# Performance work log

Measured on AMD Instinct MI355X. Metric: run time of the kernel, lower is better.

The kernel has to match this reference:

```python
import jax, jax.numpy as jnp
import numpy as np
from jax import lax

V, D, B, S = 50000, 300, 32, 128
H = 1024          # LSTM hidden per direction
NT = 9            # number of CRF tags
BN_EPS = 1e-5


def setup_inputs() -> dict:
    key = jax.random.key(0)
    ks = iter(jax.random.split(key, 48))
    def nrm(shape, scale=0.05):
        return jax.random.normal(next(ks), shape, dtype=jnp.float32) * scale
    inp = {}
    inp["x"] = jax.random.randint(next(ks), (B, S), 0, V)
    inp["y"] = jax.random.randint(next(ks), (B, S), 0, NT)
    inp["mask"] = jnp.ones((B, S), dtype=bool)
    inp["emb"] = nrm((V, D), 0.1)
    inp["lin1_w"] = nrm((512, D)); inp["lin1_b"] = jnp.zeros((512,), jnp.float32)
    in_sizes = [512, 2 * H, 2 * H, 2 * H]
    for l, isz in enumerate(in_sizes):
        inp[f"wih{l}"] = nrm((2, 4 * H, isz))   # [dir, 4H, in]
        inp[f"whh{l}"] = nrm((2, 4 * H, H))
        inp[f"bias{l}"] = jnp.zeros((2, 4 * H), jnp.float32)  # b_ih + b_hh combined
    inp["bn_gamma"] = jnp.ones((2 * H,), jnp.float32)
    inp["bn_beta"] = jnp.zeros((2 * H,), jnp.float32)
    inp["lin2_w"] = nrm((NT, 2 * H)); inp["lin2_b"] = jnp.zeros((NT,), jnp.float32)
    inp["crf_start"] = nrm((NT,), 0.1)
    inp["crf_end"] = nrm((NT,), 0.1)
    inp["crf_trans"] = nrm((NT, NT), 0.1)
    return inp


def _lstm_dir(xs, Wih, Whh, b):
    # xs: [S, B, in] -> hs: [S, B, H]; torch gate order i, f, g, o
    pre = jnp.einsum('sbi,gi->sbg', xs, Wih) + b  # [S,B,4H]
    h0 = jnp.zeros((xs.shape[1], Whh.shape[1]), xs.dtype)
    def step(carry, p):
        h, c = carry
        g = p + h @ Whh.T
        i, f, gg, o = jnp.split(g, 4, axis=-1)
        c = jax.nn.sigmoid(f) * c + jax.nn.sigmoid(i) * jnp.tanh(gg)
        h = jax.nn.sigmoid(o) * jnp.tanh(c)
        return (h, c), h
    _, hs = lax.scan(step, (h0, h0), pre)
    return hs


def _bilstm(xs, Wih, Whh, b):
    fwd = _lstm_dir(xs, Wih[0], Whh[0], b[0])
    bwd = _lstm_dir(xs[::-1], Wih[1], Whh[1], b[1])[::-1]
    return jnp.concatenate([fwd, bwd], axis=-1)


def _crf_llh(emis, tags, mask, start, end, trans):
    # torchcrf CRF forward, batch_first, reduction='sum'
    mf = mask.astype(emis.dtype)
    e_tag = jnp.take_along_axis(emis, tags[..., None], -1)[..., 0]  # [B,S]
    num = start[tags[:, 0]] + e_tag[:, 0]
    tr = trans[tags[:, :-1], tags[:, 1:]]                           # [B,S-1]
    num = num + jnp.sum(mf[:, 1:] * (tr + e_tag[:, 1:]), axis=1)
    lengths = mask.sum(axis=1).astype(jnp.int32)
    last_tag = jnp.take_along_axis(tags, (lengths - 1)[:, None], 1)[:, 0]
    num = num + end[last_tag]
    # forward algorithm (log-sum-exp recurrence over seq)
    alpha0 = start + emis[:, 0]                                     # [B,NT]
    seq_e = jnp.transpose(emis[:, 1:], (1, 0, 2))                   # [S-1,B,NT]
    seq_m = jnp.transpose(mask[:, 1:], (1, 0))                      # [S-1,B]
    def step(alpha, inp):
        e_t, m_t = inp
        nxt = jax.nn.logsumexp(alpha[:, :, None] + trans[None] + e_t[:, None, :], axis=1)
        return jnp.where(m_t[:, None], nxt, alpha), None
    alpha, _ = lax.scan(step, alpha0, (seq_e, seq_m))
    den = jax.nn.logsumexp(alpha + end, axis=1)
    return jnp.sum(num - den)


def reference(x, y, mask, emb, lin1_w, lin1_b,
              wih0, whh0, bias0, wih1, whh1, bias1,
              wih2, whh2, bias2, wih3, whh3, bias3,
              bn_gamma, bn_beta, lin2_w, lin2_b,
              crf_start, crf_end, crf_trans):
    h = emb[x]                          # [B,S,D]
    h = h @ lin1_w.T + lin1_b           # [B,S,512]
    hs = jnp.transpose(h, (1, 0, 2))    # [S,B,512]
    for Wih, Whh, bb in ((wih0, whh0, bias0), (wih1, whh1, bias1),
                         (wih2, whh2, bias2), (wih3, whh3, bias3)):
        hs = _bilstm(hs, Wih, Whh, bb)  # [S,B,2048]
    h = jnp.transpose(hs, (1, 0, 2))    # [B,S,2048]
    # BatchNorm1d eval (running mean 0, var 1) -> affine; ReLU; Dropout eval = id
    h = jax.nn.relu(bn_gamma * h / jnp.sqrt(jnp.float32(1.0 + BN_EPS)) + bn_beta)
    emis = h @ lin2_w.T + lin2_b        # [B,S,9]
    return _crf_llh(emis, y, mask, crf_start, crf_end, crf_trans)
```

## Files before the change

### kernel.cpp

```cpp
#include <hip/hip_runtime.h>
#include <hip/hip_bf16.h>

typedef __attribute__((ext_vector_type(8))) short short8;
typedef __attribute__((ext_vector_type(4))) float f32x4;
typedef unsigned short ushort_t;
typedef unsigned long long u64_t;

__device__ __forceinline__ ushort_t f2bf(float f) {
    __hip_bfloat16 h = __float2bfloat16(f);
    return *(ushort_t*)&h;
}
__device__ __forceinline__ float bf2f(ushort_t u) {
    union { float f; unsigned u32; } x; x.u32 = ((unsigned)u) << 16; return x.f;
}
__device__ __forceinline__ float sigmoidf_(float x) { return 1.0f / (1.0f + expf(-x)); }

__device__ __forceinline__ short8 cvt8(const float* p) {
    short8 r;
    #pragma unroll
    for (int j = 0; j < 8; j++) r[j] = (short)f2bf(p[j]);
    return r;
}

__global__ void lin1_pad(const float* __restrict__ w, ushort_t* __restrict__ d) {
    int idx = blockIdx.x * 256 + threadIdx.x;
    if (idx >= 512 * 320) return;
    int n = idx / 320, k = idx % 320;
    d[idx] = (k < 300) ? f2bf(w[n * 300 + k]) : (ushort_t)0;
}

__global__ void emb_gather(const int* __restrict__ x, const float* __restrict__ emb,
                           ushort_t* __restrict__ XE) {
    int tok = blockIdx.x;
    int s = tok >> 5, b = tok & 31;
    int row = x[b * 128 + s];
    const float* e = emb + (size_t)row * 300;
    for (int d = threadIdx.x; d < 320; d += 64)
        XE[(size_t)tok * 320 + d] = (d < 300) ? f2bf(e[d]) : (ushort_t)0;
}

template<bool WF32, bool F32OUT>
__global__ __launch_bounds__(256) void gemm_bias(
    const ushort_t* __restrict__ X, const void* __restrict__ Wv,
    const float* __restrict__ bias, void* __restrict__ Cv,
    int K, int ldx, int ldw, int ldc)
{
    __shared__ __align__(16) ushort_t As[4 * 64 * 8];
    __shared__ __align__(16) ushort_t Bs[4 * 64 * 8];
    const int tid = threadIdx.x;
    const int lane = tid & 63;
    const int w = tid >> 6;
    const int wm = w & 1, wn = w >> 1;
    const int m0 = blockIdx.x * 64, n0 = blockIdx.y * 64;
    const int mt = tid >> 6;
    const int r = lane & 15, q = lane >> 4;
    const ushort_t* xsrc = X + (size_t)(m0 + mt * 16 + r) * ldx + q * 8;
    const ushort_t* wsrcb = WF32 ? nullptr : (const ushort_t*)Wv + (size_t)(n0 + mt * 16 + r) * ldw + q * 8;
    const float*    wsrcf = WF32 ? (const float*)Wv + (size_t)(n0 + mt * 16 + r) * ldw + q * 8 : nullptr;
    f32x4 acc00 = {0,0,0,0}, acc01 = {0,0,0,0}, acc10 = {0,0,0,0}, acc11 = {0,0,0,0};
    for (int k0 = 0; k0 < K; k0 += 32) {
        __syncthreads();
        *(uint4*)&As[(mt * 64 + lane) * 8] = *(const uint4*)(xsrc + k0);
        if (WF32) {
            float tmp[8];
            *(float4*)&tmp[0] = *(const float4*)(wsrcf + k0);
            *(float4*)&tmp[4] = *(const float4*)(wsrcf + k0 + 4);
            *(short8*)&Bs[(mt * 64 + lane) * 8] = cvt8(tmp);
        } else {
            *(uint4*)&Bs[(mt * 64 + lane) * 8] = *(const uint4*)(wsrcb + k0);
        }
        __syncthreads();
        short8 a0 = *(const short8*)&As[((2 * wm    ) * 64 + lane) * 8];
        short8 a1 = *(const short8*)&As[((2 * wm + 1) * 64 + lane) * 8];
        short8 b0 = *(const short8*)&Bs[((2 * wn    ) * 64 + lane) * 8];
        short8 b1 = *(const short8*)&Bs[((2 * wn + 1) * 64 + lane) * 8];
        acc00 = __builtin_amdgcn_mfma_f32_16x16x32_bf16(a0, b0, acc00, 0, 0, 0);
        acc01 = __builtin_amdgcn_mfma_f32_16x16x32_bf16(a0, b1, acc01, 0, 0, 0);
        acc10 = __builtin_amdgcn_mfma_f32_16x16x32_bf16(a1, b0, acc10, 0, 0, 0);
        acc11 = __builtin_amdgcn_mfma_f32_16x16x32_bf16(a1, b1, acc11, 0, 0, 0);
    }
    const int mb = m0 + wm * 32, nb = n0 + wn * 32;
    f32x4 accs[2][2] = {{acc00, acc01}, {acc10, acc11}};
    for (int i = 0; i < 2; i++)
        for (int j = 0; j < 2; j++) {
            int n = nb + j * 16 + r;
            float bv = bias[n];
            #pragma unroll
            for (int reg = 0; reg < 4; reg++) {
                int m = mb + i * 16 + q * 4 + reg;
                float v = accs[i][j][reg] + bv;
                if (F32OUT) ((float*)Cv)[(size_t)m * ldc + n] = v;
                else ((ushort_t*)Cv)[(size_t)m * ldc + n] = f2bf(v);
            }
        }
}

__device__ __forceinline__ void gbar(unsigned* cnt, int dir, int& epoch) {
    __syncthreads();
    epoch++;
    if (threadIdx.x == 0) {
        unsigned* c = cnt + dir * 32;
        __hip_atomic_fetch_add(c, 1u, __ATOMIC_RELAXED, __HIP_MEMORY_SCOPE_AGENT);
        unsigned tgt = (unsigned)epoch * 32u;
        int spins = 0;
        while (__hip_atomic_load(c, __ATOMIC_RELAXED, __HIP_MEMORY_SCOPE_AGENT) < tgt) {
            __builtin_amdgcn_s_sleep(1);
            if (++spins >= 65536) {
                spins = 0;
                if (__hip_atomic_load(c, __ATOMIC_ACQUIRE, __HIP_MEMORY_SCOPE_AGENT) >= tgt)
                    break;
            }
        }
    }
    __syncthreads();
}

__global__ __launch_bounds__(512) void lstm_scan(
    const float* __restrict__ PRE,
    const float* __restrict__ WHH,
    ushort_t* __restrict__ H,
    ushort_t* __restrict__ OUT,
    unsigned* __restrict__ cnt,
    int epoch0)
{
    const int tid = threadIdx.x;
    const int lane = tid & 63;
    const int w = tid >> 6;
    const int dir = blockIdx.x >> 5;
    const int slice = blockIdx.x & 31;
    const int u0 = slice * 32;
    __shared__ __align__(16) ushort_t Af[2 * 32 * 64 * 8];
    __shared__ float gl[32 * 132];

    const int colw = w * 16 + (lane & 15);
    short8 bfr[32];
    {
        const int gate = colw >> 5, unit = colw & 31;
        const float* wrow = WHH + ((size_t)(dir * 4096 + gate * 1024 + u0 + unit)) * 1024 + (lane >> 4) * 8;
        #pragma unroll
        for (int kc = 0; kc < 32; kc++) {
            float tmp[8];
            *(float4*)&tmp[0] = *(const float4*)(wrow + kc * 32);
            *(float4*)&tmp[4] = *(const float4*)(wrow + kc * 32 + 4);
            bfr[kc] = cvt8(tmp);
        }
    }
    const int eb = tid >> 4, eu = tid & 15;
    float cst0 = 0.f, cst1 = 0.f;
    if ((eu & 1) == 0) {
        ushort_t* hz = H + (size_t)((0 * 2 + dir) * 32 + eb) * 1024 + u0;
        __hip_atomic_store((unsigned*)(hz + eu),      0u, __ATOMIC_RELAXED, __HIP_MEMORY_SCOPE_AGENT);
        __hip_atomic_store((unsigned*)(hz + 16 + eu), 0u, __ATOMIC_RELAXED, __HIP_MEMORY_SCOPE_AGENT);
    }
    int epoch = epoch0;
    gbar(cnt, dir, epoch);

    for (int t = 0; t < 128; t++) {
        const int s = dir ? (127 - t) : t;
        const int bufr = t & 1, bufw = bufr ^ 1;
        float pb[8];
        {
            const float* pp = PRE + ((size_t)(s * 32 + eb)) * 8192 + (size_t)dir * 4096 + u0 + eu;
            #pragma unroll
            for (int g = 0; g < 4; g++) {
                pb[2 * g]     = pp[g * 1024];
                pb[2 * g + 1] = pp[g * 1024 + 16];
            }
        }
        const ushort_t* Hsrc = H + (size_t)((bufr * 2 + dir) * 32) * 1024;
        u64_t tmp[16];
        #pragma unroll
        for (int i = 0; i < 8; i++) {
            int c = tid + i * 512;
            int ln = c & 63;
            int kc = (c >> 6) & 31;
            int mt2 = c >> 11;
            int b = mt2 * 16 + (ln & 15);
            int k = kc * 32 + (ln >> 4) * 8;
            const u64_t* src = (const u64_t*)(Hsrc + (size_t)b * 1024 + k);
            tmp[2 * i]     = __hip_atomic_load(src,     __ATOMIC_RELAXED, __HIP_MEMORY_SCOPE_AGENT);
            tmp[2 * i + 1] = __hip_atomic_load(src + 1, __ATOMIC_RELAXED, __HIP_MEMORY_SCOPE_AGENT);
        }
        #pragma unroll
        for (int i = 0; i < 8; i++) {
            int c = tid + i * 512;
            *(u64_t*)&Af[(size_t)c * 8]     = tmp[2 * i];
            *(u64_t*)&Af[(size_t)c * 8 + 4] = tmp[2 * i + 1];
        }
        __syncthreads();
        f32x4 acc0 = {0,0,0,0}, acc1 = {0,0,0,0};
        #pragma unroll
        for (int kc = 0; kc < 32; kc++) {
            short8 a0 = *(const short8*)&Af[(size_t)((     kc) * 64 + lane) * 8];
            short8 a1 = *(const short8*)&Af[(size_t)((32 + kc) * 64 + lane) * 8];
            acc0 = __builtin_amdgcn_mfma_f32_16x16x32_bf16(a0, bfr[kc], acc0, 0, 0, 0);
            acc1 = __builtin_amdgcn_mfma_f32_16x16x32_bf16(a1, bfr[kc], acc1, 0, 0, 0);
        }
        const int rowb = (lane >> 4) * 4;
        #pragma unroll
        for (int reg = 0; reg < 4; reg++) {
            gl[(rowb + reg) * 132 + colw]        = acc0[reg];
            gl[(16 + rowb + reg) * 132 + colw]   = acc1[reg];
        }
        __syncthreads();
        {
            float gi0 = gl[eb * 132 +  0 + eu] + pb[0];
            float gi1 = gl[eb * 132 + 16 + eu] + pb[1];
            float gf0 = gl[eb * 132 + 32 + eu] + pb[2];
            float gf1 = gl[eb * 132 + 48 + eu] + pb[3];
            float gg0 = gl[eb * 132 + 64 + eu] + pb[4];
            float gg1 = gl[eb * 132 + 80 + eu] + pb[5];
            float go0 = gl[eb * 132 + 96 + eu] + pb[6];
            float go1 = gl[eb * 132 + 112 + eu] + pb[7];
            cst0 = sigmoidf_(gf0) * cst0 + sigmoidf_(gi0) * tanhf(gg0);
            cst1 = sigmoidf_(gf1) * cst1 + sigmoidf_(gi1) * tanhf(gg1);
            float h0 = sigmoidf_(go0) * tanhf(cst0);
            float h1 = sigmoidf_(go1) * tanhf(cst1);
            ushort_t hb0 = f2bf(h0), hb1 = f2bf(h1);
            unsigned o0 = (unsigned)(ushort_t)__shfl_xor((int)(unsigned)hb0, 1);
            unsigned o1 = (unsigned)(ushort_t)__shfl_xor((int)(unsigned)hb1, 1);
            if ((eu & 1) == 0) {
                ushort_t* hw = H + (size_t)((bufw * 2 + dir) * 32 + eb) * 1024 + u0;
                __hip_atomic_store((unsigned*)(hw + eu),      (unsigned)hb0 | (o0 << 16),
                                   __ATOMIC_RELAXED, __HIP_MEMORY_SCOPE_AGENT);
                __hip_atomic_store((unsigned*)(hw + 16 + eu), (unsigned)hb1 | (o1 << 16),
                                   __ATOMIC_RELAXED, __HIP_MEMORY_SCOPE_AGENT);
            }
            ushort_t* op = OUT + ((size_t)(s * 32 + eb)) * 2048 + (size_t)dir * 1024 + u0;
            op[eu] = hb0;
            op[16 + eu] = hb1;
        }
        gbar(cnt, dir, epoch);
    }
}

__global__ void emis_kernel(const ushort_t* __restrict__ Xf,
                            const float* __restrict__ gamma, const float* __restrict__ beta,
                            const float* __restrict__ w2, const float* __restrict__ b2,
                            float* __restrict__ EM)
{
    int idx = blockIdx.x * 256 + threadIdx.x;
    if (idx >= 32 * 128 * 9) return;
    int k = idx % 9;
    int tok = idx / 9;
    int s = tok >> 5, b = tok & 31;
    const float inv = 0.9999950000374997f;
    float acc = b2[k];
    const ushort_t* xr = Xf + (size_t)tok * 2048;
    const float* wr = w2 + (size_t)k * 2048;
    for (int j = 0; j < 2048; j++) {
        float h = gamma[j] * bf2f(xr[j]) * inv + beta[j];
        h = h > 0.f ? h : 0.f;
        acc += h * wr[j];
    }
    EM[((size_t)b * 128 + s) * 9 + k] = acc;
}

__global__ __launch_bounds__(512) void crf_kernel(
    const float* __restrict__ EM,
    const int* __restrict__ y,
    const float* __restrict__ start, const float* __restrict__ endw,
    const float* __restrict__ trans,
    float* __restrict__ out)
{
    __shared__ float tr[81], st[9], en[9];
    __shared__ float alpha[2][32][12];
    __shared__ float numsh[32], densh[32];
    int tid = threadIdx.x;
    if (tid < 81) tr[tid] = trans[tid];
    if (tid < 9) { st[tid] = start[tid]; en[tid] = endw[tid]; }
    __syncthreads();
    if (tid < 32) {
        int b = tid;
        const int* yb = y + b * 128;
        const float* ebm = EM + (size_t)b * 1152;
        float num = st[yb[0]] + ebm[yb[0]];
        for (int s = 1; s < 128; s++)
            num += tr[yb[s - 1] * 9 + yb[s]] + ebm[s * 9 + yb[s]];
        num += en[yb[127]];
        numsh[b] = num;
    }
    int b = tid / 9, k = tid % 9;
    bool act = tid < 288;
    if (act) alpha[0][b][k] = st[k] + EM[(size_t)b * 1152 + k];
    __syncthreads();
    for (int s = 1; s < 128; s++) {
        int cur = s & 1, prv = cur ^ 1;
        if (act) {
            float m = -1e30f;
            #pragma unroll
            for (int j = 0; j < 9; j++)
                m = fmaxf(m, alpha[prv][b][j] + tr[j * 9 + k]);
            float sum = 0.f;
            #pragma unroll
            for (int j = 0; j < 9; j++)
                sum += expf(alpha[prv][b][j] + tr[j * 9 + k] - m);
            alpha[cur][b][k] = m + logf(sum) + EM[(size_t)b * 1152 + s * 9 + k];
        }
        __syncthreads();
    }
    if (tid < 32) {
        float m = -1e30f;
        for (int j = 0; j < 9; j++) m = fmaxf(m, alpha[1][tid][j] + en[j]);
        float sum = 0.f;
        for (int j = 0; j < 9; j++) sum += expf(alpha[1][tid][j] + en[j] - m);
        densh[tid] = m + logf(sum);
    }
    __syncthreads();
    if (tid == 0) {
        float tot = 0.f;
        for (int bb = 0; bb < 32; bb++) tot += numsh[bb] - densh[bb];
        out[0] = tot;
    }
}

extern "C" void kernel_launch(void* const* d_in, const int* in_sizes, int n_in,
                              void* d_out, int out_size, void* d_ws, size_t ws_size,
                              hipStream_t stream) {
    const int*   x       = (const int*)d_in[0];
    const int*   y       = (const int*)d_in[1];
    const float* emb     = (const float*)d_in[3];
    const float* lin1_w  = (const float*)d_in[4];
    const float* lin1_b  = (const float*)d_in[5];
    const float* wih[4]  = {(const float*)d_in[6],  (const float*)d_in[9],
                            (const float*)d_in[12], (const float*)d_in[15]};
    const float* whh[4]  = {(const float*)d_in[7],  (const float*)d_in[10],
                            (const float*)d_in[13], (const float*)d_in[16]};
    const float* biasl[4]= {(const float*)d_in[8],  (const float*)d_in[11],
                            (const float*)d_in[14], (const float*)d_in[17]};
    const float* bn_g    = (const float*)d_in[18];
    const float* bn_b    = (const float*)d_in[19];
    const float* lin2_w  = (const float*)d_in[20];
    const float* lin2_b  = (const float*)d_in[21];
    const float* crf_s   = (const float*)d_in[22];
    const float* crf_e   = (const float*)d_in[23];
    const float* crf_t   = (const float*)d_in[24];

    char* ws = (char*)d_ws;
    size_t off = 0;
    auto alloc = [&](size_t bytes) { size_t r = off; off += (bytes + 255) & ~(size_t)255; return r; };
    size_t oCNT  = alloc(256);
    size_t oXE   = alloc((size_t)4096 * 320 * 2);
    size_t oWL1  = alloc((size_t)512 * 320 * 2);
    size_t oXB0  = alloc((size_t)4096 * 2048 * 2);
    size_t oXB1  = alloc((size_t)4096 * 2048 * 2);
    size_t oPRE  = alloc((size_t)4096 * 8192 * 4);
    size_t oH    = alloc((size_t)2 * 2 * 32 * 1024 * 2);
    size_t oEM   = alloc((size_t)32 * 128 * 9 * 4);
    (void)ws_size; (void)in_sizes; (void)n_in; (void)out_size;

    unsigned* cnt  = (unsigned*)(ws + oCNT);
    ushort_t* XE   = (ushort_t*)(ws + oXE);
    ushort_t* WL1  = (ushort_t*)(ws + oWL1);
    ushort_t* XB0  = (ushort_t*)(ws + oXB0);
    ushort_t* XB1  = (ushort_t*)(ws + oXB1);
    float*    PRE  = (float*)(ws + oPRE);
    ushort_t* Hb   = (ushort_t*)(ws + oH);
    float*    EM   = (float*)(ws + oEM);

    hipMemsetAsync(ws + oCNT, 0, 256, stream);
    emb_gather<<<4096, 64, 0, stream>>>(x, emb, XE);
    lin1_pad<<<(512 * 320 + 255) / 256, 256, 0, stream>>>(lin1_w, WL1);
    gemm_bias<false, false><<<dim3(64, 8), 256, 0, stream>>>(XE, WL1, lin1_b, XB0, 320, 320, 320, 512);

    for (int l = 0; l < 4; l++) {
        int Kl = (l == 0) ? 512 : 2048;
        ushort_t* Xin  = (l % 2 == 0) ? XB0 : XB1;
        ushort_t* Xout = (l % 2 == 0) ? XB1 : XB0;
        gemm_bias<true, true><<<dim3(64, 128), 256, 0, stream>>>(Xin, wih[l], biasl[l], PRE,
                                                                 Kl, Kl, Kl, 8192);
        lstm_scan<<<64, 512, 0, stream>>>(PRE, whh[l], Hb, Xout, cnt, l * 129);
    }
    emis_kernel<<<144, 256, 0, stream>>>(XB0, bn_g, bn_b, lin2_w, lin2_b, EM);
    crf_kernel<<<1, 512, 0, stream>>>(EM, y, crf_s, crf_e, crf_t, (float*)d_out);
}
```

Before: 6.519 ms.

## Use per-block flag barrier, pre-convert Wih to bf16, reorder PRE loads, vectorize emis

```diff
diff --git a/kernel.cpp b/kernel.cpp
--- a/kernel.cpp
+++ b/kernel.cpp
@@ -27,6 +27,15 @@
     if (idx >= 512 * 320) return;
     int n = idx / 320, k = idx % 320;
     d[idx] = (k < 300) ? f2bf(w[n * 300 + k]) : (ushort_t)0;
+}
+
+__global__ void wcvt(const float* __restrict__ w, ushort_t* __restrict__ d, int n) {
+    int idx = (blockIdx.x * 256 + threadIdx.x) * 8;
+    if (idx >= n) return;
+    float tmp[8];
+    *(float4*)&tmp[0] = *(const float4*)(w + idx);
+    *(float4*)&tmp[4] = *(const float4*)(w + idx + 4);
+    *(short8*)&d[idx] = cvt8(tmp);
 }
 
 __global__ void emb_gather(const int* __restrict__ x, const float* __restrict__ emb,
@@ -95,20 +104,22 @@
         }
 }
 
-__device__ __forceinline__ void gbar(unsigned* cnt, int dir, int& epoch) {
+__device__ __forceinline__ void gbar(unsigned* flags, int dir, int slice, int epoch) {
     __syncthreads();
-    epoch++;
-    if (threadIdx.x == 0) {
-        unsigned* c = cnt + dir * 32;
-        __hip_atomic_fetch_add(c, 1u, __ATOMIC_RELAXED, __HIP_MEMORY_SCOPE_AGENT);
-        unsigned tgt = (unsigned)epoch * 32u;
+    if (threadIdx.x == 0)
+        __hip_atomic_store(&flags[(dir * 32 + slice) * 16], (unsigned)epoch,
+                           __ATOMIC_RELAXED, __HIP_MEMORY_SCOPE_AGENT);
+    if (threadIdx.x < 64) {
+        const unsigned* f = &flags[(dir * 32 + (threadIdx.x & 31)) * 16];
         int spins = 0;
-        while (__hip_atomic_load(c, __ATOMIC_RELAXED, __HIP_MEMORY_SCOPE_AGENT) < tgt) {
+        while (true) {
+            unsigned v = __hip_atomic_load(f, __ATOMIC_RELAXED, __HIP_MEMORY_SCOPE_AGENT);
+            if (__all(v >= (unsigned)epoch)) break;
             __builtin_amdgcn_s_sleep(1);
             if (++spins >= 65536) {
                 spins = 0;
-                if (__hip_atomic_load(c, __ATOMIC_ACQUIRE, __HIP_MEMORY_SCOPE_AGENT) >= tgt)
-                    break;
+                v = __hip_atomic_load(f, __ATOMIC_ACQUIRE, __HIP_MEMORY_SCOPE_AGENT);
+                if (__all(v >= (unsigned)epoch)) break;
             }
         }
     }
@@ -120,7 +131,7 @@
     const float* __restrict__ WHH,
     ushort_t* __restrict__ H,
     ushort_t* __restrict__ OUT,
-    unsigned* __restrict__ cnt,
+    unsigned* __restrict__ flags,
     int epoch0)
 {
     const int tid = threadIdx.x;
@@ -152,21 +163,12 @@
         __hip_atomic_store((unsigned*)(hz + eu),      0u, __ATOMIC_RELAXED, __HIP_MEMORY_SCOPE_AGENT);
         __hip_atomic_store((unsigned*)(hz + 16 + eu), 0u, __ATOMIC_RELAXED, __HIP_MEMORY_SCOPE_AGENT);
     }
-    int epoch = epoch0;
-    gbar(cnt, dir, epoch);
+    int epoch = epoch0 + 1;
+    gbar(flags, dir, slice, epoch);
 
     for (int t = 0; t < 128; t++) {
         const int s = dir ? (127 - t) : t;
         const int bufr = t & 1, bufw = bufr ^ 1;
-        float pb[8];
-        {
-            const float* pp = PRE + ((size_t)(s * 32 + eb)) * 8192 + (size_t)dir * 4096 + u0 + eu;
-            #pragma unroll
-            for (int g = 0; g < 4; g++) {
-                pb[2 * g]     = pp[g * 1024];
-                pb[2 * g + 1] = pp[g * 1024 + 16];
-            }
-        }
         const ushort_t* Hsrc = H + (size_t)((bufr * 2 + dir) * 32) * 1024;
         u64_t tmp[16];
         #pragma unroll
@@ -180,6 +182,15 @@
             const u64_t* src = (const u64_t*)(Hsrc + (size_t)b * 1024 + k);
             tmp[2 * i]     = __hip_atomic_load(src,     __ATOMIC_RELAXED, __HIP_MEMORY_SCOPE_AGENT);
             tmp[2 * i + 1] = __hip_atomic_load(src + 1, __ATOMIC_RELAXED, __HIP_MEMORY_SCOPE_AGENT);
+        }
+        float pb[8];
+        {
+            const float* pp = PRE + ((size_t)(s * 32 + eb)) * 8192 + (size_t)dir * 4096 + u0 + eu;
+            #pragma unroll
+            for (int g = 0; g < 4; g++) {
+                pb[2 * g]     = pp[g * 1024];
+                pb[2 * g + 1] = pp[g * 1024 + 16];
+            }
         }
         #pragma unroll
         for (int i = 0; i < 8; i++) {
@@ -230,30 +241,65 @@
             op[eu] = hb0;
             op[16 + eu] = hb1;
         }
-        gbar(cnt, dir, epoch);
-    }
-}
-
-__global__ void emis_kernel(const ushort_t* __restrict__ Xf,
-                            const float* __restrict__ gamma, const float* __restrict__ beta,
-                            const float* __restrict__ w2, const float* __restrict__ b2,
-                            float* __restrict__ EM)
+        epoch++;
+        gbar(flags, dir, slice, epoch);
+    }
+}
+
+__global__ __launch_bounds__(256) void emis_kernel(
+    const ushort_t* __restrict__ Xf,
+    const float* __restrict__ gamma, const float* __restrict__ beta,
+    const float* __restrict__ w2, const float* __restrict__ b2,
+    float* __restrict__ EM)
 {
-    int idx = blockIdx.x * 256 + threadIdx.x;
-    if (idx >= 32 * 128 * 9) return;
-    int k = idx % 9;
-    int tok = idx / 9;
-    int s = tok >> 5, b = tok & 31;
+    const int lane = threadIdx.x & 63;
+    const int wv = threadIdx.x >> 6;
+    const int tok = blockIdx.x * 4 + wv;
+    const int s = tok >> 5, b = tok & 31;
     const float inv = 0.9999950000374997f;
-    float acc = b2[k];
-    const ushort_t* xr = Xf + (size_t)tok * 2048;
-    const float* wr = w2 + (size_t)k * 2048;
-    for (int j = 0; j < 2048; j++) {
-        float h = gamma[j] * bf2f(xr[j]) * inv + beta[j];
-        h = h > 0.f ? h : 0.f;
-        acc += h * wr[j];
-    }
-    EM[((size_t)b * 128 + s) * 9 + k] = acc;
+    const int j0 = lane * 4;
+    float hn[32];
+    #pragma unroll
+    for (int c = 0; c < 8; c++) {
+        int j = j0 + c * 256;
+        u64_t xv = *(const u64_t*)(Xf + (size_t)tok * 2048 + j);
+        float4 gv = *(const float4*)(gamma + j);
+        float4 bv = *(const float4*)(beta + j);
+        float x0 = bf2f((ushort_t)(xv      )), x1 = bf2f((ushort_t)(xv >> 16));
+        float x2 = bf2f((ushort_t)(xv >> 32)), x3 = bf2f((ushort_t)(xv >> 48));
+        float h0 = gv.x * x0 * inv + bv.x;
+        float h1 = gv.y * x1 * inv + bv.y;
+        float h2 = gv.z * x2 * inv + bv.z;
+        float h3 = gv.w * x3 * inv + bv.w;
+        hn[c * 4 + 0] = h0 > 0.f ? h0 : 0.f;
+        hn[c * 4 + 1] = h1 > 0.f ? h1 : 0.f;
+        hn[c * 4 + 2] = h2 > 0.f ? h2 : 0.f;
+        hn[c * 4 + 3] = h3 > 0.f ? h3 : 0.f;
+    }
+    float acc[9];
+    #pragma unroll
+    for (int k = 0; k < 9; k++) {
+        const float* wr = w2 + (size_t)k * 2048 + j0;
+        float a = 0.f;
+        #pragma unroll
+        for (int c = 0; c < 8; c++) {
+            float4 wv4 = *(const float4*)(wr + c * 256);
+            a += hn[c * 4 + 0] * wv4.x + hn[c * 4 + 1] * wv4.y
+               + hn[c * 4 + 2] * wv4.z + hn[c * 4 + 3] * wv4.w;
+        }
+        acc[k] = a;
+    }
+    #pragma unroll
+    for (int k = 0; k < 9; k++) {
+        #pragma unroll
+        for (int off = 32; off > 0; off >>= 1)
+            acc[k] += __shfl_xor(acc[k], off);
+    }
+    if (lane == 0) {
+        float* em = EM + ((size_t)b * 128 + s) * 9;
+        #pragma unroll
+        for (int k = 0; k < 9; k++) em[k] = acc[k] + b2[k];
+    }
 }
 
 __global__ __launch_bounds__(512) void crf_kernel(
@@ -339,7 +385,7 @@
     char* ws = (char*)d_ws;
     size_t off = 0;
     auto alloc = [&](size_t bytes) { size_t r = off; off += (bytes + 255) & ~(size_t)255; return r; };
-    size_t oCNT  = alloc(256);
+    size_t oFLG  = alloc(4096);
     size_t oXE   = alloc((size_t)4096 * 320 * 2);
     size_t oWL1  = alloc((size_t)512 * 320 * 2);
     size_t oXB0  = alloc((size_t)4096 * 2048 * 2);
@@ -347,9 +393,10 @@
     size_t oPRE  = alloc((size_t)4096 * 8192 * 4);
     size_t oH    = alloc((size_t)2 * 2 * 32 * 1024 * 2);
     size_t oEM   = alloc((size_t)32 * 128 * 9 * 4);
+    size_t oWB   = alloc((size_t)8192 * 2048 * 2);
     (void)ws_size; (void)in_sizes; (void)n_in; (void)out_size;
 
-    unsigned* cnt  = (unsigned*)(ws + oCNT);
+    unsigned* flags = (unsigned*)(ws + oFLG);
     ushort_t* XE   = (ushort_t*)(ws + oXE);
     ushort_t* WL1  = (ushort_t*)(ws + oWL1);
     ushort_t* XB0  = (ushort_t*)(ws + oXB0);
@@ -357,8 +404,9 @@
     float*    PRE  = (float*)(ws + oPRE);
     ushort_t* Hb   = (ushort_t*)(ws + oH);
     float*    EM   = (float*)(ws + oEM);
-
-    hipMemsetAsync(ws + oCNT, 0, 256, stream);
+    ushort_t* WB   = (ushort_t*)(ws + oWB);
+
+    hipMemsetAsync(ws + oFLG, 0, 4096, stream);
     emb_gather<<<4096, 64, 0, stream>>>(x, emb, XE);
     lin1_pad<<<(512 * 320 + 255) / 256, 256, 0, stream>>>(lin1_w, WL1);
     gemm_bias<false, false><<<dim3(64, 8), 256, 0, stream>>>(XE, WL1, lin1_b, XB0, 320, 320, 320, 512);
@@ -367,10 +415,12 @@
         int Kl = (l == 0) ? 512 : 2048;
         ushort_t* Xin  = (l % 2 == 0) ? XB0 : XB1;
         ushort_t* Xout = (l % 2 == 0) ? XB1 : XB0;
-        gemm_bias<true, true><<<dim3(64, 128), 256, 0, stream>>>(Xin, wih[l], biasl[l], PRE,
-                                                                 Kl, Kl, Kl, 8192);
-        lstm_scan<<<64, 512, 0, stream>>>(PRE, whh[l], Hb, Xout, cnt, l * 129);
-    }
-    emis_kernel<<<144, 256, 0, stream>>>(XB0, bn_g, bn_b, lin2_w, lin2_b, EM);
+        int nw = 8192 * Kl;
+        wcvt<<<nw / 2048, 256, 0, stream>>>(wih[l], WB, nw);
+        gemm_bias<false, true><<<dim3(64, 128), 256, 0, stream>>>(Xin, WB, biasl[l], PRE,
+                                                                  Kl, Kl, Kl, 8192);
+        lstm_scan<<<64, 512, 0, stream>>>(PRE, whh[l], Hb, Xout, flags, l * 129);
+    }
+    emis_kernel<<<1024, 256, 0, stream>>>(XB0, bn_g, bn_b, lin2_w, lin2_b, EM);
     crf_kernel<<<1, 512, 0, stream>>>(EM, y, crf_s, crf_e, crf_t, (float*)d_out);
 }
```

Result: faster. 5.726 ms (-12.2%).
